# Kernel optimization log

Measured on AMD Instinct MI355X. Metric: run time of the kernel, lower is better.

The kernel has to match this reference:

```python
import jax, jax.numpy as jnp
import numpy as np

S, D, H, MLP = 2048, 1024, 16, 4096
DK = D // H
EPS = 1e-5  # torch LayerNorm default


def setup_inputs() -> dict:
    key = jax.random.key(0)
    ks = jax.random.split(key, 8)
    init = lambda k, shape, fan_in: jax.random.normal(k, shape, jnp.float32) * (fan_in ** -0.5)
    return {
        "x": jax.random.normal(ks[0], (S, D), jnp.float32),
        "wq": init(ks[1], (D, D), D), "bq": jnp.zeros((D,), jnp.float32),
        "wk": init(ks[2], (D, D), D), "bk": jnp.zeros((D,), jnp.float32),
        "wv": init(ks[3], (D, D), D), "bv": jnp.zeros((D,), jnp.float32),
        "wo": init(ks[4], (D, D), D), "bo": jnp.zeros((D,), jnp.float32),
        "w1": init(ks[5], (D, MLP), D), "b1": jnp.zeros((MLP,), jnp.float32),
        "w2": init(ks[6], (MLP, D), MLP), "b2": jnp.zeros((D,), jnp.float32),
        "ln1_g": jnp.ones((D,), jnp.float32), "ln1_b": jnp.zeros((D,), jnp.float32),
        "ln2_g": jnp.ones((D,), jnp.float32), "ln2_b": jnp.zeros((D,), jnp.float32),
    }


def _layernorm(x, g, b):
    m = jnp.mean(x, axis=-1, keepdims=True)
    v = jnp.var(x, axis=-1, keepdims=True)
    return (x - m) * jax.lax.rsqrt(v + EPS) * g + b


def reference(x, wq, bq, wk, bk, wv, bv, wo, bo, w1, b1, w2, b2, ln1_g, ln1_b, ln2_g, ln2_b):
    # --- residual 1: pre-LN multi-head self-attention ---
    h = _layernorm(x, ln1_g, ln1_b)
    q = (h @ wq + bq).reshape(S, H, DK).transpose(1, 0, 2)  # [H,S,DK]
    k = (h @ wk + bk).reshape(S, H, DK).transpose(1, 0, 2)
    v = (h @ wv + bv).reshape(S, H, DK).transpose(1, 0, 2)
    scores = jnp.einsum('hqd,hkd->hqk', q, k) / jnp.sqrt(jnp.float32(DK))  # [H,S,S]
    attn = jax.nn.softmax(scores, axis=-1)
    o = jnp.einsum('hqk,hkd->hqd', attn, v)  # [H,S,DK]
    # Faithful to original: x.contiguous().view(S, -1) is a raw reshape of the
    # [H,S,DK] buffer (no transpose back to [S,H,DK]).
    o = o.reshape(S, D)
    x = x + (o @ wo + bo)
    # --- residual 2: pre-LN GELU FFN ---
    h2 = _layernorm(x, ln2_g, ln2_b)
    f = jax.nn.gelu(h2 @ w1 + b1, approximate=False)  # torch nn.GELU = exact erf
    x = x + (f @ w2 + b2)
    return x
```

## Files before the change

kernel.cpp:

```cpp
#include <hip/hip_runtime.h>


constexpr int kS = 2048, kD = 1024, kH = 16, kDK = 64, kMLP = 4096;
constexpr float kEps = 1e-5f;

using u16 = unsigned short;
using u32 = unsigned int;
typedef float f32x4 __attribute__((ext_vector_type(4)));
typedef short bf16x8 __attribute__((ext_vector_type(8)));

__device__ __forceinline__ u16 f2b(float f) {
  u32 u = __builtin_bit_cast(u32, f);
  return (u16)((u + 0x7fffu + ((u >> 16) & 1u)) >> 16);
}

typedef const __attribute__((address_space(1))) u32* gas1;
typedef __attribute__((address_space(3))) u32* las3;
__device__ __forceinline__ void async16(const void* g, void* l) {
  __builtin_amdgcn_global_load_lds((gas1)g, (las3)l, 16, 0, 0);
}

__global__ __launch_bounds__(256)
void ln_kernel(const float* __restrict__ x, const float* __restrict__ g,
               const float* __restrict__ b, u16* __restrict__ out) {
  __shared__ float red[8];
  const int row = blockIdx.x, tid = threadIdx.x;
  const float4 v = *(const float4*)(x + (size_t)row * kD + tid * 4);
  float s = v.x + v.y + v.z + v.w;
  float ss = v.x * v.x + v.y * v.y + v.z * v.z + v.w * v.w;
#pragma unroll
  for (int d = 1; d < 64; d <<= 1) { s += __shfl_xor(s, d); ss += __shfl_xor(ss, d); }
  if ((tid & 63) == 0) { red[tid >> 6] = s; red[4 + (tid >> 6)] = ss; }
  __syncthreads();
  const float m = (red[0] + red[1] + red[2] + red[3]) * (1.f / kD);
  const float var = (red[4] + red[5] + red[6] + red[7]) * (1.f / kD) - m * m;
  const float r = rsqrtf(var + kEps);
  const float4 gv = *(const float4*)(g + tid * 4);
  const float4 bv = *(const float4*)(b + tid * 4);
  ushort4 o;
  o.x = f2b((v.x - m) * r * gv.x + bv.x);
  o.y = f2b((v.y - m) * r * gv.y + bv.y);
  o.z = f2b((v.z - m) * r * gv.z + bv.z);
  o.w = f2b((v.w - m) * r * gv.w + bv.w);
  *(ushort4*)(out + (size_t)row * kD + tid * 4) = o;
}

__global__ __launch_bounds__(256)
void transpose_cvt(const float* __restrict__ in, u16* __restrict__ out, int R, int C) {
  __shared__ float tile[32][33];
  const int c0 = blockIdx.x * 32, r0 = blockIdx.y * 32;
  const int x = threadIdx.x, y = threadIdx.y;
#pragma unroll
  for (int i = 0; i < 4; ++i)
    tile[y + i * 8][x] = in[(size_t)(r0 + y + i * 8) * C + c0 + x];
  __syncthreads();
#pragma unroll
  for (int i = 0; i < 4; ++i)
    out[(size_t)(c0 + y + i * 8) * R + r0 + x] = f2b(tile[x][y + i * 8]);
}

__global__ void concat_bias(const float* __restrict__ bq, const float* __restrict__ bk,
                            const float* __restrict__ bv, float* __restrict__ out) {
  int i = blockIdx.x * 256 + threadIdx.x;
  out[i] = i < kD ? bq[i] : (i < 2 * kD ? bk[i - kD] : bv[i - 2 * kD]);
}

__global__ __launch_bounds__(256)
void vtrans(const u16* __restrict__ qkv, u16* __restrict__ vt) {
  __shared__ u16 t[64][72];
  const int s0 = blockIdx.x * 64, h = blockIdx.y, tid = threadIdx.x;
#pragma unroll
  for (int r = 0; r < 2; ++r) {
    int chunk = r * 256 + tid, row = chunk >> 3, col = (chunk & 7) * 8;
    uint4 v = *(const uint4*)(qkv + (size_t)(s0 + row) * 3072 + 2 * kD + h * 64 + col);
    *(uint4*)(&t[row][col]) = v;
  }
  __syncthreads();
#pragma unroll
  for (int r = 0; r < 2; ++r) {
    int chunk = r * 256 + tid, drow = chunk >> 3, scol = (chunk & 7) * 8;
    u16 tmp[8];
#pragma unroll
    for (int j = 0; j < 8; ++j) tmp[j] = t[scol + j][drow];
    *(uint4*)(vt + (size_t)h * 64 * kS + (size_t)drow * kS + s0 + scol) = *(uint4*)tmp;
  }
}

template <int EPI>
__global__ __launch_bounds__(256, 2)
void gemm_bt(const u16* __restrict__ A, const u16* __restrict__ Bt,
             const float* __restrict__ bias, void* __restrict__ Cout,
             int N, int K, int Ksub) {
  constexpr int BM = 128, BN = 128, BK = 32;
  constexpr int MT = 4, NT = 4;
  __shared__ u16 As[BM * BK];
  __shared__ u16 Bs[BN * BK];
  const int tid = threadIdx.x;
  const int w = tid >> 6, l = tid & 63;
  const int wm = w >> 1, wn = w & 1;
  const int row0 = blockIdx.y * BM, col0 = blockIdx.x * BN;
  const int koff = blockIdx.z * Ksub;

  const int sc = ((l & 3) ^ ((l >> 3) & 3)) * 8;
  const u16* Ag = A + (size_t)(row0 + w * 16 + (l >> 2)) * K + koff + sc;
  const u16* Bg = Bt + (size_t)(col0 + w * 16 + (l >> 2)) * K + koff + sc;
  u16* AsW = As + w * 512;
  u16* BsW = Bs + w * 512;

  f32x4 acc[MT][NT] = {};
  const int q = l >> 4;

  for (int kt = 0; kt < Ksub; kt += BK) {
#pragma unroll
    for (int r = 0; r < 2; ++r) async16(Ag + (size_t)r * 64 * K + kt, AsW + r * 2048);
#pragma unroll
    for (int r = 0; r < 2; ++r) async16(Bg + (size_t)r * 64 * K + kt, BsW + r * 2048);
    __syncthreads();
    bf16x8 af[MT], bfr[NT];
#pragma unroll
    for (int i = 0; i < MT; ++i) {
      const int ra = wm * 64 + i * 16 + (l & 15);
      af[i] = *(const bf16x8*)(As + ra * 32 + (q ^ ((ra >> 1) & 3)) * 8);
    }
#pragma unroll
    for (int j = 0; j < NT; ++j) {
      const int rb = wn * 64 + j * 16 + (l & 15);
      bfr[j] = *(const bf16x8*)(Bs + rb * 32 + (q ^ ((rb >> 1) & 3)) * 8);
    }
#pragma unroll
    for (int i = 0; i < MT; ++i)
#pragma unroll
      for (int j = 0; j < NT; ++j)
        acc[i][j] = __builtin_amdgcn_mfma_f32_16x16x32_bf16(af[i], bfr[j], acc[i][j], 0, 0, 0);
    __syncthreads();
  }

  float* Pf = nullptr;
  if constexpr (EPI == 3)
    Pf = (float*)Cout + (size_t)blockIdx.z * gridDim.y * BM * N;
#pragma unroll
  for (int i = 0; i < MT; ++i) {
    const int row = row0 + wm * 64 + i * 16 + ((l >> 4) << 2);
#pragma unroll
    for (int j = 0; j < NT; ++j) {
      const int col = col0 + wn * 64 + j * 16 + (l & 15);
      float bb = 0.f;
      if constexpr (EPI != 3) bb = bias[col];
#pragma unroll
      for (int r = 0; r < 4; ++r) {
        const size_t idx = (size_t)(row + r) * N + col;
        float v = acc[i][j][r] + bb;
        if constexpr (EPI == 0) {
          ((u16*)Cout)[idx] = f2b(v);
        } else if constexpr (EPI == 1) {
          ((u16*)Cout)[idx] = f2b(0.5f * v * (1.f + erff(v * 0.7071067811865475f)));
        } else {
          Pf[idx] = v;
        }
      }
    }
  }
}

template <int KS>
__global__ __launch_bounds__(256)
void reduce_add(const float* __restrict__ parts, const float* __restrict__ bias,
                const float* __restrict__ res, float* __restrict__ out,
                int N, size_t strideMN) {
  const size_t b = ((size_t)blockIdx.x * 256 + threadIdx.x) * 4;
  float4 a = *(const float4*)(res + b);
  const float4 bv = *(const float4*)(bias + (b & (size_t)(N - 1)));
  a.x += bv.x; a.y += bv.y; a.z += bv.z; a.w += bv.w;
#pragma unroll
  for (int s = 0; s < KS; ++s) {
    const float4 p = *(const float4*)(parts + s * strideMN + b);
    a.x += p.x; a.y += p.y; a.z += p.z; a.w += p.w;
  }
  *(float4*)(out + b) = a;
}

__global__ __launch_bounds__(256, 2)
void flash_attn(const u16* __restrict__ qkv, const u16* __restrict__ vt,
                u16* __restrict__ og) {
  constexpr int LQ = 72;
  constexpr int LV = 136;
  __shared__ u16 Qs[64 * LQ];
  __shared__ u16 Ks[128 * LQ];
  __shared__ u16 Vs[64 * LV];
  __shared__ u16 Ps[4][16 * LV];
  const int tid = threadIdx.x, w = tid >> 6, l = tid & 63;
  const int h = blockIdx.y, q0 = blockIdx.x * 64;

#pragma unroll
  for (int r = 0; r < 2; ++r) {
    int chunk = r * 256 + tid, row = chunk >> 3, col = (chunk & 7) * 8;
    uint4 v = *(const uint4*)(qkv + (size_t)(q0 + row) * 3072 + h * 64 + col);
    *(uint4*)(&Qs[row * LQ + col]) = v;
  }
  __syncthreads();
  bf16x8 qa[2];
#pragma unroll
  for (int kq = 0; kq < 2; ++kq)
    qa[kq] = *(const bf16x8*)(&Qs[(w * 16 + (l & 15)) * LQ + kq * 32 + (l >> 4) * 8]);

  f32x4 oacc[4] = {};
  float mi[4], li[4];
#pragma unroll
  for (int r = 0; r < 4; ++r) { mi[r] = -1e30f; li[r] = 0.f; }

  for (int kt = 0; kt < kS; kt += 128) {
    __syncthreads();
#pragma unroll
    for (int r = 0; r < 4; ++r) {
      int chunk = r * 256 + tid, row = chunk >> 3, col = (chunk & 7) * 8;
      uint4 v = *(const uint4*)(qkv + (size_t)(kt + row) * 3072 + kD + h * 64 + col);
      *(uint4*)(&Ks[row * LQ + col]) = v;
    }
#pragma unroll
    for (int r = 0; r < 4; ++r) {
      int chunk = r * 256 + tid, row = chunk >> 4, col = (chunk & 15) * 8;
      uint4 v = *(const uint4*)(vt + (size_t)h * 64 * kS + (size_t)row * kS + kt + col);
      *(uint4*)(&Vs[row * LV + col]) = v;
    }
    __syncthreads();

    f32x4 s[8];
#pragma unroll
    for (int n = 0; n < 8; ++n) {
      f32x4 z = {};
      bf16x8 kb0 = *(const bf16x8*)(&Ks[(n * 16 + (l & 15)) * LQ + (l >> 4) * 8]);
      bf16x8 kb1 = *(const bf16x8*)(&Ks[(n * 16 + (l & 15)) * LQ + 32 + (l >> 4) * 8]);
      z = __builtin_amdgcn_mfma_f32_16x16x32_bf16(qa[0], kb0, z, 0, 0, 0);
      z = __builtin_amdgcn_mfma_f32_16x16x32_bf16(qa[1], kb1, z, 0, 0, 0);
      s[n] = z;
    }
    float alpha[4];
#pragma unroll
    for (int r = 0; r < 4; ++r) {
      float m = -1e30f;
#pragma unroll
      for (int n = 0; n < 8; ++n) m = fmaxf(m, s[n][r]);
#pragma unroll
      for (int d = 1; d < 16; d <<= 1) m = fmaxf(m, __shfl_xor(m, d));
      m *= 0.125f;
      float mn = fmaxf(mi[r], m);
      alpha[r] = __expf(mi[r] - mn);
      mi[r] = mn;
      li[r] *= alpha[r];
    }
#pragma unroll
    for (int n = 0; n < 4; ++n)
#pragma unroll
      for (int r = 0; r < 4; ++r) oacc[n][r] *= alpha[r];
    float rs[4] = {0.f, 0.f, 0.f, 0.f};
#pragma unroll
    for (int n = 0; n < 8; ++n)
#pragma unroll
      for (int r = 0; r < 4; ++r) {
        float pv = __expf(s[n][r] * 0.125f - mi[r]);
        rs[r] += pv;
        Ps[w][((l >> 4) * 4 + r) * LV + n * 16 + (l & 15)] = f2b(pv);
      }
#pragma unroll
    for (int r = 0; r < 4; ++r) {
      float t = rs[r];
#pragma unroll
      for (int d = 1; d < 16; d <<= 1) t += __shfl_xor(t, d);
      li[r] += t;
    }
    bf16x8 pa[4];
#pragma unroll
    for (int ks = 0; ks < 4; ++ks)
      pa[ks] = *(const bf16x8*)(&Ps[w][(l & 15) * LV + ks * 32 + (l >> 4) * 8]);
#pragma unroll
    for (int n = 0; n < 4; ++n)
#pragma unroll
      for (int ks = 0; ks < 4; ++ks) {
        bf16x8 vb = *(const bf16x8*)(&Vs[(n * 16 + (l & 15)) * LV + ks * 32 + (l >> 4) * 8]);
        oacc[n] = __builtin_amdgcn_mfma_f32_16x16x32_bf16(pa[ks], vb, oacc[n], 0, 0, 0);
      }
  }
#pragma unroll
  for (int r = 0; r < 4; ++r) {
    float inv = 1.f / li[r];
    int srow = q0 + w * 16 + (l >> 4) * 4 + r;
#pragma unroll
    for (int n = 0; n < 4; ++n) {
      int d = n * 16 + (l & 15);
      og[(size_t)h * kS * kDK + (size_t)srow * kDK + d] = f2b(oacc[n][r] * inv);
    }
  }
}

extern "C" void kernel_launch(void* const* d_in, const int* in_sizes, int n_in,
                              void* d_out, int out_size, void* d_ws, size_t ws_size,
                              hipStream_t stream) {
  const float* x = (const float*)d_in[0];
  const float* wq = (const float*)d_in[1];
  const float* bq = (const float*)d_in[2];
  const float* wk = (const float*)d_in[3];
  const float* bk = (const float*)d_in[4];
  const float* wv = (const float*)d_in[5];
  const float* bv = (const float*)d_in[6];
  const float* wo = (const float*)d_in[7];
  const float* bo = (const float*)d_in[8];
  const float* w1 = (const float*)d_in[9];
  const float* b1 = (const float*)d_in[10];
  const float* w2 = (const float*)d_in[11];
  const float* b2 = (const float*)d_in[12];
  const float* ln1g = (const float*)d_in[13];
  const float* ln1b = (const float*)d_in[14];
  const float* ln2g = (const float*)d_in[15];
  const float* ln2b = (const float*)d_in[16];
  float* out = (float*)d_out;

  char* p = (char*)d_ws;
  auto alloc = [&](size_t bytes) { void* q = (void*)p; p += (bytes + 255) & ~(size_t)255; return q; };
  u16* h1 = (u16*)alloc((size_t)kS * kD * 2);
  u16* wqkvt = (u16*)alloc((size_t)3 * kD * kD * 2);
  u16* qkv = (u16*)alloc((size_t)kS * 3 * kD * 2);
  u16* vt = (u16*)alloc((size_t)kH * kDK * kS * 2);
  u16* og = (u16*)alloc((size_t)kS * kD * 2);
  u16* wot = (u16*)alloc((size_t)kD * kD * 2);
  u16* h2 = (u16*)alloc((size_t)kS * kD * 2);
  u16* w1t = (u16*)alloc((size_t)kD * kMLP * 2);
  float* bqkv = (float*)alloc((size_t)3 * kD * 4);
  float* x2 = (float*)alloc((size_t)kS * kD * 4);
  u16* fbuf = (u16*)alloc((size_t)kS * kMLP * 2);
  u16* w2t = (u16*)alloc((size_t)kMLP * kD * 2);
  float* part = (float*)d_ws;
  const size_t strideMN = (size_t)kS * kD;

  dim3 tb(32, 8);
  transpose_cvt<<<dim3(kD / 32, kD / 32), tb, 0, stream>>>(wq, wqkvt, kD, kD);
  transpose_cvt<<<dim3(kD / 32, kD / 32), tb, 0, stream>>>(wk, wqkvt + kD * kD, kD, kD);
  transpose_cvt<<<dim3(kD / 32, kD / 32), tb, 0, stream>>>(wv, wqkvt + 2 * kD * kD, kD, kD);
  transpose_cvt<<<dim3(kD / 32, kD / 32), tb, 0, stream>>>(wo, wot, kD, kD);
  transpose_cvt<<<dim3(kMLP / 32, kD / 32), tb, 0, stream>>>(w1, w1t, kD, kMLP);
  transpose_cvt<<<dim3(kD / 32, kMLP / 32), tb, 0, stream>>>(w2, w2t, kMLP, kD);
  concat_bias<<<dim3(12), dim3(256), 0, stream>>>(bq, bk, bv, bqkv);

  ln_kernel<<<dim3(kS), dim3(256), 0, stream>>>(x, ln1g, ln1b, h1);
  gemm_bt<0><<<dim3(3 * kD / 128, kS / 128, 1), dim3(256), 0, stream>>>(
      h1, wqkvt, bqkv, qkv, 3 * kD, kD, kD);
  vtrans<<<dim3(kS / 64, kH), dim3(256), 0, stream>>>(qkv, vt);
  flash_attn<<<dim3(kS / 64, kH), dim3(256), 0, stream>>>(qkv, vt, og);
  gemm_bt<3><<<dim3(kD / 128, kS / 128, 2), dim3(256), 0, stream>>>(
      og, wot, nullptr, part, kD, kD, kD / 2);
  reduce_add<2><<<dim3(kS * kD / 4 / 256), dim3(256), 0, stream>>>(
      part, bo, x, x2, kD, strideMN);
  ln_kernel<<<dim3(kS), dim3(256), 0, stream>>>(x2, ln2g, ln2b, h2);
  gemm_bt<1><<<dim3(kMLP / 128, kS / 128, 1), dim3(256), 0, stream>>>(
      h2, w1t, b1, fbuf, kMLP, kD, kD);
  gemm_bt<3><<<dim3(kD / 128, kS / 128, 4), dim3(256), 0, stream>>>(
      fbuf, w2t, nullptr, part, kD, kMLP, kMLP / 4);
  reduce_add<4><<<dim3(kS * kD / 4 / 256), dim3(256), 0, stream>>>(
      part, b2, x2, out, kD, strideMN);
}
```

Before: 317.3 us.

## Prefetch next K/V tile into registers and transpose S tile in flash attention

```diff
diff --git a/kernel.cpp b/kernel.cpp
--- a/kernel.cpp
+++ b/kernel.cpp
@@ -189,6 +189,7 @@
   __shared__ u16 Vs[64 * LV];
   __shared__ u16 Ps[4][16 * LV];
   const int tid = threadIdx.x, w = tid >> 6, l = tid & 63;
+  const int t4 = l >> 4, ln = l & 15;
   const int h = blockIdx.y, q0 = blockIdx.x * 64;
 
 #pragma unroll
@@ -197,96 +198,119 @@
     uint4 v = *(const uint4*)(qkv + (size_t)(q0 + row) * 3072 + h * 64 + col);
     *(uint4*)(&Qs[row * LQ + col]) = v;
   }
+  uint4 kreg[4], vreg[4];
+#pragma unroll
+  for (int r = 0; r < 4; ++r) {
+    int chunk = r * 256 + tid, row = chunk >> 3, col = (chunk & 7) * 8;
+    kreg[r] = *(const uint4*)(qkv + (size_t)row * 3072 + kD + h * 64 + col);
+  }
+#pragma unroll
+  for (int r = 0; r < 4; ++r) {
+    int chunk = r * 256 + tid, row = chunk >> 4, col = (chunk & 15) * 8;
+    vreg[r] = *(const uint4*)(vt + (size_t)h * 64 * kS + (size_t)row * kS + col);
+  }
   __syncthreads();
   bf16x8 qa[2];
 #pragma unroll
   for (int kq = 0; kq < 2; ++kq)
-    qa[kq] = *(const bf16x8*)(&Qs[(w * 16 + (l & 15)) * LQ + kq * 32 + (l >> 4) * 8]);
+    qa[kq] = *(const bf16x8*)(&Qs[(w * 16 + ln) * LQ + kq * 32 + t4 * 8]);
 
   f32x4 oacc[4] = {};
-  float mi[4], li[4];
-#pragma unroll
-  for (int r = 0; r < 4; ++r) { mi[r] = -1e30f; li[r] = 0.f; }
+  float mi = -1e30f, li = 0.f;
 
   for (int kt = 0; kt < kS; kt += 128) {
-    __syncthreads();
 #pragma unroll
     for (int r = 0; r < 4; ++r) {
       int chunk = r * 256 + tid, row = chunk >> 3, col = (chunk & 7) * 8;
-      uint4 v = *(const uint4*)(qkv + (size_t)(kt + row) * 3072 + kD + h * 64 + col);
-      *(uint4*)(&Ks[row * LQ + col]) = v;
+      *(uint4*)(&Ks[row * LQ + col]) = kreg[r];
     }
 #pragma unroll
     for (int r = 0; r < 4; ++r) {
       int chunk = r * 256 + tid, row = chunk >> 4, col = (chunk & 15) * 8;
-      uint4 v = *(const uint4*)(vt + (size_t)h * 64 * kS + (size_t)row * kS + kt + col);
-      *(uint4*)(&Vs[row * LV + col]) = v;
+      *(uint4*)(&Vs[row * LV + col]) = vreg[r];
     }
     __syncthreads();
-
-    f32x4 s[8];
+    if (kt + 128 < kS) {
+#pragma unroll
+      for (int r = 0; r < 4; ++r) {
+        int chunk = r * 256 + tid, row = chunk >> 3, col = (chunk & 7) * 8;
+        kreg[r] = *(const uint4*)(qkv + (size_t)(kt + 128 + row) * 3072 + kD + h * 64 + col);
+      }
+#pragma unroll
+      for (int r = 0; r < 4; ++r) {
+        int chunk = r * 256 + tid, row = chunk >> 4, col = (chunk & 15) * 8;
+        vreg[r] = *(const uint4*)(vt + (size_t)h * 64 * kS + (size_t)row * kS + kt + 128 + col);
+      }
+    }
+
+    f32x4 st[8];
 #pragma unroll
     for (int n = 0; n < 8; ++n) {
       f32x4 z = {};
-      bf16x8 kb0 = *(const bf16x8*)(&Ks[(n * 16 + (l & 15)) * LQ + (l >> 4) * 8]);
-      bf16x8 kb1 = *(const bf16x8*)(&Ks[(n * 16 + (l & 15)) * LQ + 32 + (l >> 4) * 8]);
-      z = __builtin_amdgcn_mfma_f32_16x16x32_bf16(qa[0], kb0, z, 0, 0, 0);
-      z = __builtin_amdgcn_mfma_f32_16x16x32_bf16(qa[1], kb1, z, 0, 0, 0);
-      s[n] = z;
-    }
-    float alpha[4];
-#pragma unroll
-    for (int r = 0; r < 4; ++r) {
-      float m = -1e30f;
-#pragma unroll
-      for (int n = 0; n < 8; ++n) m = fmaxf(m, s[n][r]);
-#pragma unroll
-      for (int d = 1; d < 16; d <<= 1) m = fmaxf(m, __shfl_xor(m, d));
-      m *= 0.125f;
-      float mn = fmaxf(mi[r], m);
-      alpha[r] = __expf(mi[r] - mn);
-      mi[r] = mn;
-      li[r] *= alpha[r];
-    }
+      bf16x8 kb0 = *(const bf16x8*)(&Ks[(n * 16 + ln) * LQ + t4 * 8]);
+      bf16x8 kb1 = *(const bf16x8*)(&Ks[(n * 16 + ln) * LQ + 32 + t4 * 8]);
+      z = __builtin_amdgcn_mfma_f32_16x16x32_bf16(kb0, qa[0], z, 0, 0, 0);
+      z = __builtin_amdgcn_mfma_f32_16x16x32_bf16(kb1, qa[1], z, 0, 0, 0);
+      st[n] = z;
+    }
+    float pm = -1e30f;
+#pragma unroll
+    for (int n = 0; n < 8; ++n) {
+      float m01 = fmaxf(st[n][0], st[n][1]);
+      float m23 = fmaxf(st[n][2], st[n][3]);
+      pm = fmaxf(pm, fmaxf(m01, m23));
+    }
+    pm = fmaxf(pm, __shfl_xor(pm, 16));
+    pm = fmaxf(pm, __shfl_xor(pm, 32));
+    pm *= 0.125f;
+    const float mn = fmaxf(mi, pm);
+    const float al = __expf(mi - mn);
+    mi = mn;
+    li *= al;
+    float ar[4];
+#pragma unroll
+    for (int r = 0; r < 4; ++r) ar[r] = __shfl(al, t4 * 4 + r);
 #pragma unroll
     for (int n = 0; n < 4; ++n)
 #pragma unroll
-      for (int r = 0; r < 4; ++r) oacc[n][r] *= alpha[r];
-    float rs[4] = {0.f, 0.f, 0.f, 0.f};
-#pragma unroll
-    for (int n = 0; n < 8; ++n)
-#pragma unroll
-      for (int r = 0; r < 4; ++r) {
-        float pv = __expf(s[n][r] * 0.125f - mi[r]);
-        rs[r] += pv;
-        Ps[w][((l >> 4) * 4 + r) * LV + n * 16 + (l & 15)] = f2b(pv);
-      }
-#pragma unroll
-    for (int r = 0; r < 4; ++r) {
-      float t = rs[r];
-#pragma unroll
-      for (int d = 1; d < 16; d <<= 1) t += __shfl_xor(t, d);
-      li[r] += t;
-    }
+      for (int r = 0; r < 4; ++r) oacc[n][r] *= ar[r];
+    float ls = 0.f;
+#pragma unroll
+    for (int n = 0; n < 8; ++n) {
+      float p0 = __expf(st[n][0] * 0.125f - mi);
+      float p1 = __expf(st[n][1] * 0.125f - mi);
+      float p2 = __expf(st[n][2] * 0.125f - mi);
+      float p3 = __expf(st[n][3] * 0.125f - mi);
+      ls += (p0 + p1) + (p2 + p3);
+      uint2 pk;
+      pk.x = (u32)f2b(p0) | ((u32)f2b(p1) << 16);
+      pk.y = (u32)f2b(p2) | ((u32)f2b(p3) << 16);
+      *(uint2*)(&Ps[w][ln * LV + n * 16 + t4 * 4]) = pk;
+    }
+    ls += __shfl_xor(ls, 16);
+    ls += __shfl_xor(ls, 32);
+    li += ls;
     bf16x8 pa[4];
 #pragma unroll
     for (int ks = 0; ks < 4; ++ks)
-      pa[ks] = *(const bf16x8*)(&Ps[w][(l & 15) * LV + ks * 32 + (l >> 4) * 8]);
+      pa[ks] = *(const bf16x8*)(&Ps[w][ln * LV + ks * 32 + t4 * 8]);
 #pragma unroll
     for (int n = 0; n < 4; ++n)
 #pragma unroll
       for (int ks = 0; ks < 4; ++ks) {
-        bf16x8 vb = *(const bf16x8*)(&Vs[(n * 16 + (l & 15)) * LV + ks * 32 + (l >> 4) * 8]);
+        bf16x8 vb = *(const bf16x8*)(&Vs[(n * 16 + ln) * LV + ks * 32 + t4 * 8]);
         oacc[n] = __builtin_amdgcn_mfma_f32_16x16x32_bf16(pa[ks], vb, oacc[n], 0, 0, 0);
       }
+    __syncthreads();
   }
 #pragma unroll
   for (int r = 0; r < 4; ++r) {
-    float inv = 1.f / li[r];
-    int srow = q0 + w * 16 + (l >> 4) * 4 + r;
+    float lr = __shfl(li, t4 * 4 + r);
+    float inv = 1.f / lr;
+    int srow = q0 + w * 16 + t4 * 4 + r;
 #pragma unroll
     for (int n = 0; n < 4; ++n) {
-      int d = n * 16 + (l & 15);
+      int d = n * 16 + ln;
       og[(size_t)h * kS * kDK + (size_t)srow * kDK + d] = f2b(oacc[n][r] * inv);
     }
   }
```

Result: slower. 333.9 us (+5.2%).

## Double-buffer GEMM LDS loads and shrink tile to 128x64 for more occupancy

Applied to the files above, without the earlier changes.

```diff
diff --git a/kernel.cpp b/kernel.cpp
--- a/kernel.cpp
+++ b/kernel.cpp
@@ -87,52 +87,63 @@
 }
 
 template <int EPI>
-__global__ __launch_bounds__(256, 2)
+__global__ __launch_bounds__(256, 4)
 void gemm_bt(const u16* __restrict__ A, const u16* __restrict__ Bt,
              const float* __restrict__ bias, void* __restrict__ Cout,
              int N, int K, int Ksub) {
-  constexpr int BM = 128, BN = 128, BK = 32;
-  constexpr int MT = 4, NT = 4;
-  __shared__ u16 As[BM * BK];
-  __shared__ u16 Bs[BN * BK];
+  constexpr int BM = 128, BN = 64, BK = 32;
+  constexpr int MT = 2, NT = 4;
+  __shared__ u16 As[2][BM * BK];
+  __shared__ u16 Bs[2][BN * BK];
   const int tid = threadIdx.x;
   const int w = tid >> 6, l = tid & 63;
-  const int wm = w >> 1, wn = w & 1;
   const int row0 = blockIdx.y * BM, col0 = blockIdx.x * BN;
   const int koff = blockIdx.z * Ksub;
 
   const int sc = ((l & 3) ^ ((l >> 3) & 3)) * 8;
-  const u16* Ag = A + (size_t)(row0 + w * 16 + (l >> 2)) * K + koff + sc;
+  const u16* Ag = A + (size_t)(row0 + w * 32 + (l >> 2)) * K + koff + sc;
   const u16* Bg = Bt + (size_t)(col0 + w * 16 + (l >> 2)) * K + koff + sc;
-  u16* AsW = As + w * 512;
-  u16* BsW = Bs + w * 512;
 
   f32x4 acc[MT][NT] = {};
   const int q = l >> 4;
-
-  for (int kt = 0; kt < Ksub; kt += BK) {
-#pragma unroll
-    for (int r = 0; r < 2; ++r) async16(Ag + (size_t)r * 64 * K + kt, AsW + r * 2048);
-#pragma unroll
-    for (int r = 0; r < 2; ++r) async16(Bg + (size_t)r * 64 * K + kt, BsW + r * 2048);
-    __syncthreads();
+  const int nIter = Ksub / BK;
+
+  async16(Ag, &As[0][w * 1024]);
+  async16(Ag + (size_t)16 * K, &As[0][w * 1024 + 512]);
+  async16(Bg, &Bs[0][w * 512]);
+
+  for (int t = 0; t < nIter; ++t) {
+    const int cur = t & 1;
+    if (t + 1 < nIter) {
+      const int kt = (t + 1) * BK;
+      async16(Ag + kt, &As[cur ^ 1][w * 1024]);
+      async16(Ag + (size_t)16 * K + kt, &As[cur ^ 1][w * 1024 + 512]);
+      async16(Bg + kt, &Bs[cur ^ 1][w * 512]);
+      asm volatile("s_waitcnt vmcnt(3)" ::: "memory");
+    } else {
+      asm volatile("s_waitcnt vmcnt(0)" ::: "memory");
+    }
+    __builtin_amdgcn_s_barrier();
+    __builtin_amdgcn_sched_barrier(0);
+    const u16* Asc = As[cur];
+    const u16* Bsc = Bs[cur];
     bf16x8 af[MT], bfr[NT];
 #pragma unroll
     for (int i = 0; i < MT; ++i) {
-      const int ra = wm * 64 + i * 16 + (l & 15);
-      af[i] = *(const bf16x8*)(As + ra * 32 + (q ^ ((ra >> 1) & 3)) * 8);
+      const int ra = w * 32 + i * 16 + (l & 15);
+      af[i] = *(const bf16x8*)(Asc + ra * 32 + (q ^ ((ra >> 1) & 3)) * 8);
     }
 #pragma unroll
     for (int j = 0; j < NT; ++j) {
-      const int rb = wn * 64 + j * 16 + (l & 15);
-      bfr[j] = *(const bf16x8*)(Bs + rb * 32 + (q ^ ((rb >> 1) & 3)) * 8);
+      const int rb = j * 16 + (l & 15);
+      bfr[j] = *(const bf16x8*)(Bsc + rb * 32 + (q ^ ((rb >> 1) & 3)) * 8);
     }
 #pragma unroll
     for (int i = 0; i < MT; ++i)
 #pragma unroll
       for (int j = 0; j < NT; ++j)
         acc[i][j] = __builtin_amdgcn_mfma_f32_16x16x32_bf16(af[i], bfr[j], acc[i][j], 0, 0, 0);
-    __syncthreads();
+    __builtin_amdgcn_s_barrier();
   }
 
   float* Pf = nullptr;
@@ -140,10 +151,10 @@
     Pf = (float*)Cout + (size_t)blockIdx.z * gridDim.y * BM * N;
 #pragma unroll
   for (int i = 0; i < MT; ++i) {
-    const int row = row0 + wm * 64 + i * 16 + ((l >> 4) << 2);
+    const int row = row0 + w * 32 + i * 16 + ((l >> 4) << 2);
 #pragma unroll
     for (int j = 0; j < NT; ++j) {
-      const int col = col0 + wn * 64 + j * 16 + (l & 15);
+      const int col = col0 + j * 16 + (l & 15);
       float bb = 0.f;
       if constexpr (EPI != 3) bb = bias[col];
 #pragma unroll
@@ -341,18 +352,18 @@
   concat_bias<<<dim3(12), dim3(256), 0, stream>>>(bq, bk, bv, bqkv);
 
   ln_kernel<<<dim3(kS), dim3(256), 0, stream>>>(x, ln1g, ln1b, h1);
-  gemm_bt<0><<<dim3(3 * kD / 128, kS / 128, 1), dim3(256), 0, stream>>>(
+  gemm_bt<0><<<dim3(3 * kD / 64, kS / 128, 1), dim3(256), 0, stream>>>(
       h1, wqkvt, bqkv, qkv, 3 * kD, kD, kD);
   vtrans<<<dim3(kS / 64, kH), dim3(256), 0, stream>>>(qkv, vt);
   flash_attn<<<dim3(kS / 64, kH), dim3(256), 0, stream>>>(qkv, vt, og);
-  gemm_bt<3><<<dim3(kD / 128, kS / 128, 2), dim3(256), 0, stream>>>(
+  gemm_bt<3><<<dim3(kD / 64, kS / 128, 2), dim3(256), 0, stream>>>(
       og, wot, nullptr, part, kD, kD, kD / 2);
   reduce_add<2><<<dim3(kS * kD / 4 / 256), dim3(256), 0, stream>>>(
       part, bo, x, x2, kD, strideMN);
   ln_kernel<<<dim3(kS), dim3(256), 0, stream>>>(x2, ln2g, ln2b, h2);
-  gemm_bt<1><<<dim3(kMLP / 128, kS / 128, 1), dim3(256), 0, stream>>>(
+  gemm_bt<1><<<dim3(kMLP / 64, kS / 128, 1), dim3(256), 0, stream>>>(
       h2, w1t, b1, fbuf, kMLP, kD, kD);
-  gemm_bt<3><<<dim3(kD / 128, kS / 128, 4), dim3(256), 0, stream>>>(
+  gemm_bt<3><<<dim3(kD / 64, kS / 128, 4), dim3(256), 0, stream>>>(
       fbuf, w2t, nullptr, part, kD, kMLP, kMLP / 4);
   reduce_add<4><<<dim3(kS * kD / 4 / 256), dim3(256), 0, stream>>>(
       part, b2, x2, out, kD, strideMN);
```

Result: no change. 322.5 us (+1.6%).

## Rewrite GEMM with 128x256 tiles, BK=64 and triple-buffered async LDS pipeline

Applied to the files above, without the earlier changes.

```diff
diff --git a/kernel.cpp b/kernel.cpp
--- a/kernel.cpp
+++ b/kernel.cpp
@@ -87,63 +87,85 @@
 }
 
 template <int EPI>
-__global__ __launch_bounds__(256, 2)
+__global__ __launch_bounds__(512, 1)
 void gemm_bt(const u16* __restrict__ A, const u16* __restrict__ Bt,
              const float* __restrict__ bias, void* __restrict__ Cout,
              int N, int K, int Ksub) {
-  constexpr int BM = 128, BN = 128, BK = 32;
-  constexpr int MT = 4, NT = 4;
-  __shared__ u16 As[BM * BK];
-  __shared__ u16 Bs[BN * BK];
+  constexpr int BM = 128, BN = 256, BK = 64;
+  __shared__ u16 As[3][BM * BK];
+  __shared__ u16 Bs[3][BN * BK];
   const int tid = threadIdx.x;
   const int w = tid >> 6, l = tid & 63;
-  const int wm = w >> 1, wn = w & 1;
+  const int wm = w >> 2, wn = w & 3;
+  const int ln = l & 15, q = l >> 4;
   const int row0 = blockIdx.y * BM, col0 = blockIdx.x * BN;
   const int koff = blockIdx.z * Ksub;
-
-  const int sc = ((l & 3) ^ ((l >> 3) & 3)) * 8;
-  const u16* Ag = A + (size_t)(row0 + w * 16 + (l >> 2)) * K + koff + sc;
-  const u16* Bg = Bt + (size_t)(col0 + w * 16 + (l >> 2)) * K + koff + sc;
-  u16* AsW = As + w * 512;
-  u16* BsW = Bs + w * 512;
-
-  f32x4 acc[MT][NT] = {};
-  const int q = l >> 4;
-
-  for (int kt = 0; kt < Ksub; kt += BK) {
-#pragma unroll
-    for (int r = 0; r < 2; ++r) async16(Ag + (size_t)r * 64 * K + kt, AsW + r * 2048);
-#pragma unroll
-    for (int r = 0; r < 2; ++r) async16(Bg + (size_t)r * 64 * K + kt, BsW + r * 2048);
-    __syncthreads();
-    bf16x8 af[MT], bfr[NT];
-#pragma unroll
-    for (int i = 0; i < MT; ++i) {
-      const int ra = wm * 64 + i * 16 + (l & 15);
-      af[i] = *(const bf16x8*)(As + ra * 32 + (q ^ ((ra >> 1) & 3)) * 8);
-    }
-#pragma unroll
-    for (int j = 0; j < NT; ++j) {
-      const int rb = wn * 64 + j * 16 + (l & 15);
-      bfr[j] = *(const bf16x8*)(Bs + rb * 32 + (q ^ ((rb >> 1) & 3)) * 8);
-    }
-#pragma unroll
-    for (int i = 0; i < MT; ++i)
-#pragma unroll
-      for (int j = 0; j < NT; ++j)
-        acc[i][j] = __builtin_amdgcn_mfma_f32_16x16x32_bf16(af[i], bfr[j], acc[i][j], 0, 0, 0);
-    __syncthreads();
+  const int nIter = Ksub / BK;
+
+  const int rS = tid >> 3;
+  const int cS = ((tid & 7) ^ (rS & 7)) * 8;
+  const u16* Ab0 = A + (size_t)(row0 + rS) * K + koff + cS;
+  const u16* Bb0 = Bt + (size_t)(col0 + rS) * K + koff + cS;
+  const int dW = w * 512;
+
+  f32x4 acc[4][4] = {};
+
+  auto stage = [&](int t, int b) {
+    const int kt = t * BK;
+    async16(Ab0 + kt, &As[b][dW]);
+    async16(Ab0 + (size_t)64 * K + kt, &As[b][4096 + dW]);
+    async16(Bb0 + kt, &Bs[b][dW]);
+    async16(Bb0 + (size_t)64 * K + kt, &Bs[b][4096 + dW]);
+    async16(Bb0 + (size_t)128 * K + kt, &Bs[b][8192 + dW]);
+    async16(Bb0 + (size_t)192 * K + kt, &Bs[b][12288 + dW]);
+  };
+
+  stage(0, 0);
+  stage(1, 1);
+  asm volatile("s_waitcnt vmcnt(6)" ::: "memory");
+  __builtin_amdgcn_s_barrier();
+  __builtin_amdgcn_sched_barrier(0);
+
+  int bR = 0, bW = 2;
+  for (int t = 0; t < nIter; ++t) {
+    if (t + 2 < nIter) stage(t + 2, bW);
+    const u16* Ar = As[bR];
+    const u16* Br = Bs[bR];
+#pragma unroll
+    for (int ks = 0; ks < 2; ++ks) {
+      const int ch = ((ks * 4 + q) ^ (ln & 7)) * 8;
+      bf16x8 af[4], bf[4];
+#pragma unroll
+      for (int i = 0; i < 4; ++i)
+        af[i] = *(const bf16x8*)(Ar + (wm * 64 + i * 16 + ln) * 64 + ch);
+#pragma unroll
+      for (int j = 0; j < 4; ++j)
+        bf[j] = *(const bf16x8*)(Br + (wn * 64 + j * 16 + ln) * 64 + ch);
+      __builtin_amdgcn_s_setprio(1);
+#pragma unroll
+      for (int i = 0; i < 4; ++i)
+#pragma unroll
+        for (int j = 0; j < 4; ++j)
+          acc[i][j] = __builtin_amdgcn_mfma_f32_16x16x32_bf16(af[i], bf[j], acc[i][j], 0, 0, 0);
+      __builtin_amdgcn_s_setprio(0);
+    }
+    if (t + 2 < nIter) asm volatile("s_waitcnt vmcnt(6)" ::: "memory");
+    else               asm volatile("s_waitcnt vmcnt(0)" ::: "memory");
+    __builtin_amdgcn_s_barrier();
+    __builtin_amdgcn_sched_barrier(0);
+    bR = bR == 2 ? 0 : bR + 1;
+    bW = bW == 2 ? 0 : bW + 1;
   }
 
   float* Pf = nullptr;
   if constexpr (EPI == 3)
     Pf = (float*)Cout + (size_t)blockIdx.z * gridDim.y * BM * N;
 #pragma unroll
-  for (int i = 0; i < MT; ++i) {
-    const int row = row0 + wm * 64 + i * 16 + ((l >> 4) << 2);
-#pragma unroll
-    for (int j = 0; j < NT; ++j) {
-      const int col = col0 + wn * 64 + j * 16 + (l & 15);
+  for (int i = 0; i < 4; ++i) {
+    const int row = row0 + wm * 64 + i * 16 + q * 4;
+#pragma unroll
+    for (int j = 0; j < 4; ++j) {
+      const int col = col0 + wn * 64 + j * 16 + ln;
       float bb = 0.f;
       if constexpr (EPI != 3) bb = bias[col];
 #pragma unroll
@@ -341,18 +363,18 @@
   concat_bias<<<dim3(12), dim3(256), 0, stream>>>(bq, bk, bv, bqkv);
 
   ln_kernel<<<dim3(kS), dim3(256), 0, stream>>>(x, ln1g, ln1b, h1);
-  gemm_bt<0><<<dim3(3 * kD / 128, kS / 128, 1), dim3(256), 0, stream>>>(
+  gemm_bt<0><<<dim3(3 * kD / 256, kS / 128, 1), dim3(512), 0, stream>>>(
       h1, wqkvt, bqkv, qkv, 3 * kD, kD, kD);
   vtrans<<<dim3(kS / 64, kH), dim3(256), 0, stream>>>(qkv, vt);
   flash_attn<<<dim3(kS / 64, kH), dim3(256), 0, stream>>>(qkv, vt, og);
-  gemm_bt<3><<<dim3(kD / 128, kS / 128, 2), dim3(256), 0, stream>>>(
+  gemm_bt<3><<<dim3(kD / 256, kS / 128, 2), dim3(512), 0, stream>>>(
       og, wot, nullptr, part, kD, kD, kD / 2);
   reduce_add<2><<<dim3(kS * kD / 4 / 256), dim3(256), 0, stream>>>(
       part, bo, x, x2, kD, strideMN);
   ln_kernel<<<dim3(kS), dim3(256), 0, stream>>>(x2, ln2g, ln2b, h2);
-  gemm_bt<1><<<dim3(kMLP / 128, kS / 128, 1), dim3(256), 0, stream>>>(
+  gemm_bt<1><<<dim3(kMLP / 256, kS / 128, 1), dim3(512), 0, stream>>>(
       h2, w1t, b1, fbuf, kMLP, kD, kD);
-  gemm_bt<3><<<dim3(kD / 128, kS / 128, 4), dim3(256), 0, stream>>>(
+  gemm_bt<3><<<dim3(kD / 256, kS / 128, 4), dim3(512), 0, stream>>>(
       fbuf, w2t, nullptr, part, kD, kMLP, kMLP / 4);
   reduce_add<4><<<dim3(kS * kD / 4 / 256), dim3(256), 0, stream>>>(
       part, b2, x2, out, kD, strideMN);
```

New measurement: 320.1 us. No clear change (+0.9%).
